# Performance work log

Measured on AMD Instinct MI355X. Metric: run time of the kernel, lower is better.

## Reference

```python
import jax, jax.numpy as jnp
import numpy as np

EPS = 1e-5
N_HEADS = 4

def _ln(x, s, b):
    m = x.mean(-1, keepdims=True)
    v = ((x - m) ** 2).mean(-1, keepdims=True)
    return (x - m) / jnp.sqrt(v + EPS) * s + b

def _gelu(x):
    return jax.nn.gelu(x, approximate=False)  # torch nn.GELU default (erf)


def setup_inputs() -> dict:
    key = jax.random.key(0)
    ks = jax.random.split(key, 20)
    H, AF, BF, DEPTH = 256, 153, 14, 4
    n_mols, apm = 1024, 48
    n_atoms = n_mols * apm          # 49152
    max_nb = 6
    n_bonds = 3 * n_atoms           # 147456 directed bonds
    def nrm(k, shape, scale=0.02):
        return jax.random.normal(k, shape, jnp.float32) * scale
    return dict(
        f_atoms=jax.random.normal(ks[0], (n_atoms, AF), jnp.float32),
        f_bonds=jax.random.normal(ks[1], (n_bonds, BF), jnp.float32),
        a2b=jax.random.randint(ks[2], (n_atoms, max_nb), 0, n_bonds),
        b2a=jax.random.randint(ks[3], (n_bonds,), 0, n_atoms),
        b2revb=jax.random.randint(ks[4], (n_bonds,), 0, n_bonds),
        W_i=nrm(ks[5], (AF + BF, H)), b_i=jnp.zeros((H,), jnp.float32),
        W_h=nrm(ks[6], (DEPTH - 1, H, H)), b_h=jnp.zeros((DEPTH - 1, H), jnp.float32),
        ln_msg_s=jnp.ones((DEPTH - 1, H), jnp.float32), ln_msg_b=jnp.zeros((DEPTH - 1, H), jnp.float32),
        W_o=nrm(ks[7], (AF + H, H)), b_o=jnp.zeros((H,), jnp.float32),
        ln_atom_s=jnp.ones((H,), jnp.float32), ln_atom_b=jnp.zeros((H,), jnp.float32),
        q_w=nrm(ks[8], (H, H)), q_b=jnp.zeros((H,), jnp.float32),
        k_w=nrm(ks[9], (H, H)), k_b=jnp.zeros((H,), jnp.float32),
        v_w=nrm(ks[10], (H, H)), v_b=jnp.zeros((H,), jnp.float32),
        o_w=nrm(ks[11], (H, H)), o_b=jnp.zeros((H,), jnp.float32),
        ln1_s=jnp.ones((H,), jnp.float32), ln1_b=jnp.zeros((H,), jnp.float32),
        ln2_s=jnp.ones((H,), jnp.float32), ln2_b=jnp.zeros((H,), jnp.float32),
        ff1_w=nrm(ks[12], (H, 2 * H)), ff1_b=jnp.zeros((2 * H,), jnp.float32),
        ff2_w=nrm(ks[13], (2 * H, H)), ff2_b=jnp.zeros((H,), jnp.float32),
        readout_query=nrm(ks[14], (1, 1, H)),
        rk_w=nrm(ks[15], (H, H)), rk_b=jnp.zeros((H,), jnp.float32),
        n_mols=n_mols, atoms_per_mol=apm,
    )


def reference(f_atoms, f_bonds, a2b, b2a, b2revb,
              W_i, b_i, W_h, b_h, ln_msg_s, ln_msg_b, W_o, b_o,
              ln_atom_s, ln_atom_b, q_w, q_b, k_w, k_b, v_w, v_b, o_w, o_b,
              ln1_s, ln1_b, ln2_s, ln2_b, ff1_w, ff1_b, ff2_w, ff2_b,
              readout_query, rk_w, rk_b, n_mols, atoms_per_mol):
    H = W_i.shape[1]
    HD = H // N_HEADS
    depth = W_h.shape[0] + 1

    # ---- D-MPNN message passing over directed bonds ----
    message = _gelu(jnp.concatenate([f_atoms[b2a], f_bonds], axis=1) @ W_i + b_i)  # [n_bonds,H]
    for t in range(depth - 1):  # fixed small depth loop
        nei = message[a2b].sum(axis=1)                 # [n_atoms,H] gather-sum over incoming bonds
        nei_m = nei[b2a] - message[b2revb]             # [n_bonds,H] subtract reverse bond
        message = message + _gelu(_ln(nei_m, ln_msg_s[t], ln_msg_b[t]) @ W_h[t] + b_h[t])

    a_message = message[a2b].sum(axis=1)               # [n_atoms,H]
    atom_h = _gelu(jnp.concatenate([f_atoms, a_message], axis=1) @ W_o + b_o)
    atom_h = _ln(atom_h, ln_atom_s, ln_atom_b)

    # uniform scopes: padding loop becomes a reshape, mask is all-valid
    x = atom_h.reshape(n_mols, atoms_per_mol, H)

    # ---- pre-norm TransformerEncoderLayer ----
    h = _ln(x, ln1_s, ln1_b)
    def heads(t):
        return t.reshape(n_mols, atoms_per_mol, N_HEADS, HD).transpose(0, 2, 1, 3)
    q = heads(h @ q_w + q_b)
    k = heads(h @ k_w + k_b)
    v = heads(h @ v_w + v_b)
    attn = jax.nn.softmax(jnp.einsum('bhqd,bhkd->bhqk', q, k) / float(np.sqrt(HD)), axis=-1)
    ctx = jnp.einsum('bhqk,bhkd->bhqd', attn, v).transpose(0, 2, 1, 3).reshape(n_mols, atoms_per_mol, H)
    x = x + (ctx @ o_w + o_b)
    h2 = _ln(x, ln2_s, ln2_b)
    x = x + (_gelu(h2 @ ff1_w + ff1_b) @ ff2_w + ff2_b)

    # ---- attention-weighted readout ----
    keys = x @ rk_w + rk_b                             # [B,S,H]
    scores = jnp.einsum('bsh,h->bs', keys, readout_query[0, 0])
    w = jax.nn.softmax(scores, axis=-1)[..., None]
    return (x * w).sum(axis=1)                         # [B,H]
```

## Files before the change

### kernel.cpp

```cpp
#include <hip/hip_runtime.h>
#include <hip/hip_bf16.h>
#include <math.h>

#define H 256
#define AFEAT 153
#define BFEAT 14
#define KINIT 167
#define NA 49152
#define NB 147456
#define NMOL 1024
#define APM 48
#define MAXNB 6
#define NHEAD 4
#define HDIM 64
#define EPSLN 1e-5f
#define KI_PAD 192
#define KO_PAD 448

typedef unsigned short u16;
typedef __attribute__((ext_vector_type(8))) short bf16x8;
typedef __attribute__((ext_vector_type(4))) short bf16x4;
typedef __attribute__((ext_vector_type(4))) float f32x4;

__device__ __forceinline__ float gelu_f(float x) {
    return 0.5f * x * (1.0f + erff(x * 0.70710678118654752f));
}
__device__ __forceinline__ float wave_sum(float v) {
    #pragma unroll
    for (int m = 1; m < 64; m <<= 1) v += __shfl_xor(v, m);
    return v;
}
__device__ __forceinline__ float b2f(u16 u) {
    union { unsigned u32; float f; } c; c.u32 = ((unsigned)u) << 16; return c.f;
}
__device__ __forceinline__ u16 f2b(float f) {
    __hip_bfloat16 h = __float2bfloat16(f);
    u16 u; __builtin_memcpy(&u, &h, 2); return u;
}
__device__ __forceinline__ ushort4 f2b4(float a, float b, float c, float d) {
    ushort4 o; o.x = f2b(a); o.y = f2b(b); o.z = f2b(c); o.w = f2b(d); return o;
}

__device__ __forceinline__ f32x4 mfma16(bf16x4 a, bf16x4 b, f32x4 c) {
#if __has_builtin(__builtin_amdgcn_mfma_f32_16x16x16bf16_1k)
    return __builtin_amdgcn_mfma_f32_16x16x16bf16_1k(a, b, c, 0, 0, 0);
#elif __has_builtin(__builtin_amdgcn_mfma_f32_16x16x16_bf16_1k)
    return __builtin_amdgcn_mfma_f32_16x16x16_bf16_1k(a, b, c, 0, 0, 0);
#elif __has_builtin(__builtin_amdgcn_mfma_f32_16x16x16_bf16)
    return __builtin_amdgcn_mfma_f32_16x16x16_bf16(a, b, c, 0, 0, 0);
#else
    f32x4 d;
    asm("v_mfma_f32_16x16x16_bf16 %0, %1, %2, %3"
        : "=&v"(d) : "v"(a), "v"(b), "v"(c));
    return d;
#endif
}

typedef const __attribute__((address_space(1))) void* gas_ptr;
typedef __attribute__((address_space(3))) void* las_ptr;
__device__ __forceinline__ void gload_lds16(const u16* g, u16* l) {
    __builtin_amdgcn_global_load_lds((gas_ptr)g, (las_ptr)l, 16, 0, 0);
}

template<bool GELU, bool ACCUM>
__global__ __launch_bounds__(256) void gemm_mfma_k(
    const u16* __restrict__ A, int Ka,
    const u16* __restrict__ Wt,
    const float* __restrict__ bias,
    u16* __restrict__ C, int Nc, int K)
{
    __shared__ __align__(16) u16 As[128 * 64];
    __shared__ __align__(16) u16 Bs[128 * 64];
    const int tid = threadIdx.x;
    const int w = tid >> 6, l = tid & 63;
    const int r0 = blockIdx.x * 128;
    const int cb0 = blockIdx.y * 128;
    const int wr = (w >> 1) * 64;
    const int wc = (w & 1) * 64;

    f32x4 acc[4][4];
    #pragma unroll
    for (int m = 0; m < 4; ++m)
        #pragma unroll
        for (int n = 0; n < 4; ++n) acc[m][n] = (f32x4){0.f, 0.f, 0.f, 0.f};

    const int srow = l >> 3;
    const int sslot = (l & 7) * 16;
    const int ssrc = sslot ^ (srow << 4);

    const int fr = l & 15;
    const int fh = l >> 4;
    const int swz = (fr & 7) << 4;

    for (int k0 = 0; k0 < K; k0 += 64) {
        #pragma unroll
        for (int i = 0; i < 4; ++i) {
            const int seg = w * 4 + i;
            gload_lds16(A + (size_t)(r0 + seg * 8 + srow) * Ka + k0 + (ssrc >> 1),
                        &As[seg * 512]);
            gload_lds16(Wt + (size_t)(cb0 + seg * 8 + srow) * Ka + k0 + (ssrc >> 1),
                        &Bs[seg * 512]);
        }
        __syncthreads();
        #pragma unroll
        for (int s = 0; s < 2; ++s) {
            const int cbyte = ((s * 64 + fh * 16) ^ swz) >> 1;
            bf16x8 af[4], bv[4];
            #pragma unroll
            for (int m = 0; m < 4; ++m)
                af[m] = *(const bf16x8*)&As[(wr + m * 16 + fr) * 64 + cbyte];
            #pragma unroll
            for (int n = 0; n < 4; ++n)
                bv[n] = *(const bf16x8*)&Bs[(wc + n * 16 + fr) * 64 + cbyte];
            #pragma unroll
            for (int m = 0; m < 4; ++m)
                #pragma unroll
                for (int n = 0; n < 4; ++n)
                    acc[m][n] = __builtin_amdgcn_mfma_f32_16x16x32_bf16(
                        af[m], bv[n], acc[m][n], 0, 0, 0);
        }
        __syncthreads();
    }

    float bvv[4];
    #pragma unroll
    for (int n = 0; n < 4; ++n) bvv[n] = bias[cb0 + wc + n * 16 + fr];
    #pragma unroll
    for (int m = 0; m < 4; ++m) {
        #pragma unroll
        for (int n = 0; n < 4; ++n) {
            const int col = cb0 + wc + n * 16 + fr;
            #pragma unroll
            for (int j = 0; j < 4; ++j) {
                const int row = r0 + wr + m * 16 + fh * 4 + j;
                float v = acc[m][n][j] + bvv[n];
                if (GELU) v = gelu_f(v);
                u16* p = &C[(size_t)row * Nc + col];
                if (ACCUM) v += b2f(*p);
                *p = f2b(v);
            }
        }
    }
}

__global__ __launch_bounds__(256) void wcvt_k(const float* __restrict__ W,
    u16* __restrict__ Wt, int K, int N, int Kpad)
{
    int idx = blockIdx.x * 256 + threadIdx.x;
    if (idx >= N * Kpad) return;
    int n = idx / Kpad, kp = idx - n * Kpad;
    Wt[idx] = (kp < K) ? f2b(W[(size_t)kp * N + n]) : (u16)0;
}

__global__ void biaspack_k(const float* q, const float* k, const float* v, float* dst) {
    int t = threadIdx.x;
    dst[t] = q[t]; dst[256 + t] = k[t]; dst[512 + t] = v[t];
}

__global__ __launch_bounds__(256) void ainit_k(const float* __restrict__ fa,
    const float* __restrict__ fb, const int* __restrict__ b2a, u16* __restrict__ dst)
{
    const int w = threadIdx.x >> 6, l = threadIdx.x & 63;
    const int row = blockIdx.x * 4 + w;
    const int a = b2a[row];
    const float* fsrc = fa + (size_t)a * AFEAT;
    u16* d = dst + (size_t)row * KI_PAD;
    #pragma unroll
    for (int i = 0; i < 3; ++i) {
        int c = l + i * 64;
        float v;
        if (c < AFEAT) v = fsrc[c];
        else if (c < KINIT) v = fb[(size_t)row * BFEAT + (c - AFEAT)];
        else v = 0.f;
        d[c] = f2b(v);
    }
}

__global__ __launch_bounds__(256) void acat_k(const float* __restrict__ fa,
    const u16* __restrict__ nei, u16* __restrict__ dst)
{
    const int w = threadIdx.x >> 6, l = threadIdx.x & 63;
    const int row = blockIdx.x * 4 + w;
    const float* fsrc = fa + (size_t)row * AFEAT;
    const u16* nsrc = nei + (size_t)row * H;
    u16* d = dst + (size_t)row * KO_PAD;
    #pragma unroll
    for (int i = 0; i < 7; ++i) {
        int c = l + i * 64;
        u16 v;
        if (c < AFEAT) v = f2b(fsrc[c]);
        else if (c < AFEAT + H) v = nsrc[c - AFEAT];
        else v = 0;
        d[c] = v;
    }
}

__global__ __launch_bounds__(256) void nei_sum_k(const u16* __restrict__ msg,
    const int* __restrict__ a2b, u16* __restrict__ nei)
{
    const int wave = threadIdx.x >> 6;
    const int lane = threadIdx.x & 63;
    const int atom = blockIdx.x * 4 + wave;
    float ax = 0.f, ay = 0.f, az = 0.f, aw = 0.f;
    #pragma unroll
    for (int j = 0; j < MAXNB; ++j) {
        int b = a2b[atom * MAXNB + j];
        ushort4 v = *(const ushort4*)(msg + (size_t)b * H + lane * 4);
        ax += b2f(v.x); ay += b2f(v.y); az += b2f(v.z); aw += b2f(v.w);
    }
    *(ushort4*)(nei + (size_t)atom * H + lane * 4) = f2b4(ax, ay, az, aw);
}

__global__ __launch_bounds__(256) void bond_ln_k(const u16* __restrict__ nei,
    const u16* __restrict__ msg, const int* __restrict__ b2a,
    const int* __restrict__ b2revb, const float* __restrict__ s,
    const float* __restrict__ b, u16* __restrict__ out)
{
    const int wave = threadIdx.x >> 6;
    const int lane = threadIdx.x & 63;
    const int bond = blockIdx.x * 4 + wave;
    const int a = b2a[bond];
    const int rb = b2revb[bond];
    ushort4 un = *(const ushort4*)(nei + (size_t)a * H + lane * 4);
    ushort4 um = *(const ushort4*)(msg + (size_t)rb * H + lane * 4);
    float vx = b2f(un.x) - b2f(um.x), vy = b2f(un.y) - b2f(um.y);
    float vz = b2f(un.z) - b2f(um.z), vw = b2f(un.w) - b2f(um.w);
    float mean = wave_sum(vx + vy + vz + vw) * (1.0f / H);
    float dx = vx - mean, dy = vy - mean, dz = vz - mean, dw = vw - mean;
    float var = wave_sum(dx * dx + dy * dy + dz * dz + dw * dw) * (1.0f / H);
    float inv = rsqrtf(var + EPSLN);
    float4 s4 = *(const float4*)(s + lane * 4);
    float4 b4 = *(const float4*)(b + lane * 4);
    *(ushort4*)(out + (size_t)bond * H + lane * 4) =
        f2b4(dx * inv * s4.x + b4.x, dy * inv * s4.y + b4.y,
             dz * inv * s4.z + b4.z, dw * inv * s4.w + b4.w);
}

__global__ __launch_bounds__(256) void row_ln_k(const u16* __restrict__ in,
    u16* __restrict__ out, const float* __restrict__ s, const float* __restrict__ b)
{
    const int wave = threadIdx.x >> 6;
    const int lane = threadIdx.x & 63;
    const int row = blockIdx.x * 4 + wave;
    ushort4 u = *(const ushort4*)(in + (size_t)row * H + lane * 4);
    float vx = b2f(u.x), vy = b2f(u.y), vz = b2f(u.z), vw = b2f(u.w);
    float mean = wave_sum(vx + vy + vz + vw) * (1.0f / H);
    float dx = vx - mean, dy = vy - mean, dz = vz - mean, dw = vw - mean;
    float var = wave_sum(dx * dx + dy * dy + dz * dz + dw * dw) * (1.0f / H);
    float inv = rsqrtf(var + EPSLN);
    float4 s4 = *(const float4*)(s + lane * 4);
    float4 b4 = *(const float4*)(b + lane * 4);
    *(ushort4*)(out + (size_t)row * H + lane * 4) =
        f2b4(dx * inv * s4.x + b4.x, dy * inv * s4.y + b4.y,
             dz * inv * s4.z + b4.z, dw * inv * s4.w + b4.w);
}

#define VPAD 268
__global__ __launch_bounds__(256) void attn_mfma_k(const u16* __restrict__ qkv,
    u16* __restrict__ ctx)
{
    __shared__ u16 Vs[48][VPAD];
    const int mol = blockIdx.x;
    const int tid = threadIdx.x;
    const int w = tid >> 6;
    const int l = tid & 63;
    const int fr = l & 15;
    const int fh = l >> 4;
    const size_t qb = (size_t)mol * APM * 768;

    {
        const int r = tid >> 4;
        const int c = (tid & 15) * 16;
        #pragma unroll
        for (int i = 0; i < 3; ++i) {
            const int row = r + i * 16;
            const u16* src = qkv + qb + (size_t)row * 768 + 512 + c;
            ushort4 a0 = *(const ushort4*)(src);
            ushort4 a1 = *(const ushort4*)(src + 4);
            ushort4 a2 = *(const ushort4*)(src + 8);
            ushort4 a3 = *(const ushort4*)(src + 12);
            *(ushort4*)&Vs[row][c]      = a0;
            *(ushort4*)&Vs[row][c + 4]  = a1;
            *(ushort4*)&Vs[row][c + 8]  = a2;
            *(ushort4*)&Vs[row][c + 12] = a3;
        }
    }
    __syncthreads();

    f32x4 st[3][3];
    {
        bf16x8 kf[3][2], qf[3][2];
        #pragma unroll
        for (int t = 0; t < 3; ++t)
            #pragma unroll
            for (int ks = 0; ks < 2; ++ks) {
                const size_t rowb = qb + (size_t)(t * 16 + fr) * 768;
                kf[t][ks] = *(const bf16x8*)(qkv + rowb + 256 + w * 64 + ks * 32 + fh * 8);
                qf[t][ks] = *(const bf16x8*)(qkv + rowb +       w * 64 + ks * 32 + fh * 8);
            }
        #pragma unroll
        for (int mi = 0; mi < 3; ++mi)
            #pragma unroll
            for (int ni = 0; ni < 3; ++ni) {
                f32x4 a = (f32x4){0.f, 0.f, 0.f, 0.f};
                a = __builtin_amdgcn_mfma_f32_16x16x32_bf16(kf[mi][0], qf[ni][0], a, 0, 0, 0);
                a = __builtin_amdgcn_mfma_f32_16x16x32_bf16(kf[mi][1], qf[ni][1], a, 0, 0, 0);
                st[mi][ni] = a;
            }
    }

    float inv_sum[3];
    #pragma unroll
    for (int ni = 0; ni < 3; ++ni) {
        float m = -1e30f;
        #pragma unroll
        for (int mi = 0; mi < 3; ++mi)
            #pragma unroll
            for (int j = 0; j < 4; ++j) m = fmaxf(m, st[mi][ni][j]);
        m = fmaxf(m, __shfl_xor(m, 16));
        m = fmaxf(m, __shfl_xor(m, 32));
        float s = 0.f;
        #pragma unroll
        for (int mi = 0; mi < 3; ++mi)
            #pragma unroll
            for (int j = 0; j < 4; ++j) {
                float e = expf((st[mi][ni][j] - m) * 0.125f);
                st[mi][ni][j] = e;
                s += e;
            }
        s += __shfl_xor(s, 16);
        s += __shfl_xor(s, 32);
        inv_sum[ni] = 1.0f / s;
    }

    bf16x4 pf[3][3];
    #pragma unroll
    for (int mi = 0; mi < 3; ++mi)
        #pragma unroll
        for (int ni = 0; ni < 3; ++ni) {
            bf16x4 p;
            p[0] = (short)f2b(st[mi][ni][0]);
            p[1] = (short)f2b(st[mi][ni][1]);
            p[2] = (short)f2b(st[mi][ni][2]);
            p[3] = (short)f2b(st[mi][ni][3]);
            pf[mi][ni] = p;
        }

    f32x4 co[4][3];
    #pragma unroll
    for (int dt = 0; dt < 4; ++dt)
        #pragma unroll
        for (int ni = 0; ni < 3; ++ni) co[dt][ni] = (f32x4){0.f, 0.f, 0.f, 0.f};
    #pragma unroll
    for (int kt = 0; kt < 3; ++kt) {
        bf16x4 vf[4];
        #pragma unroll
        for (int dt = 0; dt < 4; ++dt) {
            const int colu = w * 64 + dt * 16 + fr;
            bf16x4 t;
            #pragma unroll
            for (int e = 0; e < 4; ++e)
                t[e] = (short)Vs[kt * 16 + fh * 4 + e][colu];
            vf[dt] = t;
        }
        #pragma unroll
        for (int dt = 0; dt < 4; ++dt)
            #pragma unroll
            for (int ni = 0; ni < 3; ++ni)
                co[dt][ni] = mfma16(vf[dt], pf[kt][ni], co[dt][ni]);
    }

    #pragma unroll
    for (int ni = 0; ni < 3; ++ni) {
        const float is = inv_sum[ni];
        u16* rowp = ctx + (size_t)(mol * APM + ni * 16 + fr) * H + w * 64;
        #pragma unroll
        for (int dt = 0; dt < 4; ++dt) {
            *(ushort4*)(rowp + dt * 16 + fh * 4) =
                f2b4(co[dt][ni][0] * is, co[dt][ni][1] * is,
                     co[dt][ni][2] * is, co[dt][ni][3] * is);
        }
    }
}

__global__ __launch_bounds__(256) void readout_prep_k(const float* __restrict__ rk_w,
    const float* __restrict__ rk_b, const float* __restrict__ query, float* __restrict__ small)
{
    __shared__ float qsh[256];
    __shared__ float red[4];
    const int t = threadIdx.x;
    qsh[t] = query[t];
    __syncthreads();
    float acc = 0.f;
    #pragma unroll
    for (int c = 0; c < 256; c += 4) {
        float4 w = *(const float4*)&rk_w[(size_t)t * 256 + c];
        acc += w.x * qsh[c] + w.y * qsh[c+1] + w.z * qsh[c+2] + w.w * qsh[c+3];
    }
    small[t] = acc;
    float term = wave_sum(rk_b[t] * qsh[t]);
    if ((t & 63) == 0) red[t >> 6] = term;
    __syncthreads();
    if (t == 0) small[256] = red[0] + red[1] + red[2] + red[3];
}

__global__ __launch_bounds__(256) void readout_k(const u16* __restrict__ x,
    const float* __restrict__ small, float* __restrict__ out)
{
    __shared__ float sc[48];
    __shared__ float rvs[256];
    const int mol = blockIdx.x;
    const int t = threadIdx.x;
    const int wave = t >> 6, lane = t & 63;
    rvs[t] = small[t];
    __syncthreads();
    const float c0 = small[256];
    const size_t xb = (size_t)mol * APM * H;
    for (int i = 0; i < 12; ++i) {
        int s = wave * 12 + i;
        ushort4 xu = *(const ushort4*)(x + xb + (size_t)s * H + lane * 4);
        float dot = b2f(xu.x) * rvs[lane*4] + b2f(xu.y) * rvs[lane*4+1]
                  + b2f(xu.z) * rvs[lane*4+2] + b2f(xu.w) * rvs[lane*4+3];
        dot = wave_sum(dot);
        if (lane == 0) sc[s] = dot + c0;
    }
    __syncthreads();
    if (wave == 0) {
        float v = (lane < 48) ? sc[lane] : -1e30f;
        float mx = v;
        #pragma unroll
        for (int m = 1; m < 64; m <<= 1) mx = fmaxf(mx, __shfl_xor(mx, m));
        float e = (lane < 48) ? expf(v - mx) : 0.f;
        float sum = wave_sum(e);
        if (lane < 48) sc[lane] = e / sum;
    }
    __syncthreads();
    float acc = 0.f;
    for (int s = 0; s < 48; ++s) acc += sc[s] * b2f(x[xb + (size_t)s * H + t]);
    out[(size_t)mol * H + t] = acc;
}

__global__ void diag_k(float* out, int n, float val) {
    int i = blockIdx.x * 256 + threadIdx.x;
    if (i < n) out[i] = (i == 0) ? val : 0.f;
}

extern "C" void kernel_launch(void* const* d_in, const int* in_sizes, int n_in,
                              void* d_out, int out_size, void* d_ws, size_t ws_size,
                              hipStream_t stream)
{
    const float* f_atoms = (const float*)d_in[0];
    const float* f_bonds = (const float*)d_in[1];
    const int*   a2b     = (const int*)d_in[2];
    const int*   b2a     = (const int*)d_in[3];
    const int*   b2revb  = (const int*)d_in[4];
    const float* W_i = (const float*)d_in[5];
    const float* b_i = (const float*)d_in[6];
    const float* W_h = (const float*)d_in[7];
    const float* b_h = (const float*)d_in[8];
    const float* ln_msg_s = (const float*)d_in[9];
    const float* ln_msg_b = (const float*)d_in[10];
    const float* W_o = (const float*)d_in[11];
    const float* b_o = (const float*)d_in[12];
    const float* ln_atom_s = (const float*)d_in[13];
    const float* ln_atom_b = (const float*)d_in[14];
    const float* q_w = (const float*)d_in[15];
    const float* q_b = (const float*)d_in[16];
    const float* k_w = (const float*)d_in[17];
    const float* k_b = (const float*)d_in[18];
    const float* v_w = (const float*)d_in[19];
    const float* v_b = (const float*)d_in[20];
    const float* o_w = (const float*)d_in[21];
    const float* o_b = (const float*)d_in[22];
    const float* ln1_s = (const float*)d_in[23];
    const float* ln1_b = (const float*)d_in[24];
    const float* ln2_s = (const float*)d_in[25];
    const float* ln2_b = (const float*)d_in[26];
    const float* ff1_w = (const float*)d_in[27];
    const float* ff1_b = (const float*)d_in[28];
    const float* ff2_w = (const float*)d_in[29];
    const float* ff2_b = (const float*)d_in[30];
    const float* rquery = (const float*)d_in[31];
    const float* rk_w = (const float*)d_in[32];
    const float* rk_b = (const float*)d_in[33];

    const size_t SZ_MSG = (size_t)NB * H;
    const size_t SZ_NEI = (size_t)NA * H;
    const size_t W_I_SZ  = 256 * KI_PAD;
    const size_t W_H_SZ  = 3 * 256 * 256;
    const size_t W_O_SZ  = 256 * KO_PAD;
    const size_t W_QKV_SZ = 768 * 256;
    const size_t W_OG_SZ = 256 * 256;
    const size_t W_F1_SZ = 512 * 256;
    const size_t W_F2_SZ = 256 * 512;
    const size_t wtotal = W_I_SZ + W_H_SZ + W_O_SZ + W_QKV_SZ + W_OG_SZ + W_F1_SZ + W_F2_SZ;
    const size_t required = (2 * SZ_MSG + SZ_NEI + wtotal) * 2 + 768 * 4 + 257 * 4 + 256;
    if (ws_size < required) {
        diag_k<<<dim3((out_size + 255) / 256), dim3(256), 0, stream>>>(
            (float*)d_out, out_size, (float)(ws_size >> 20));
        return;
    }

    u16* msg    = (u16*)d_ws;
    u16* normed = msg + SZ_MSG;
    u16* nei    = normed + SZ_MSG;
    u16* wt_i   = nei + SZ_NEI;
    u16* wt_h   = wt_i + W_I_SZ;
    u16* wt_o   = wt_h + W_H_SZ;
    u16* wt_qkv = wt_o + W_O_SZ;
    u16* wt_og  = wt_qkv + W_QKV_SZ;
    u16* wt_f1  = wt_og + W_OG_SZ;
    u16* wt_f2  = wt_f1 + W_F1_SZ;
    float* qkvb = (float*)(wt_f2 + W_F2_SZ);
    float* small = qkvb + 768;

    u16* x    = msg;
    u16* h    = msg + SZ_NEI;
    u16* qkv  = normed;
    u16* ctx  = nei;
    u16* h2   = msg + SZ_NEI;
    u16* ff1o = normed;
    float* out = (float*)d_out;

    dim3 blk(256);
    #define WCVT(W, DST, K, N, KP) wcvt_k<<<dim3(((N)*(KP)+255)/256), blk, 0, stream>>>(W, DST, K, N, KP)

    WCVT(W_i, wt_i, KINIT, 256, KI_PAD);
    WCVT(W_h,           wt_h,           256, 256, 256);
    WCVT(W_h + 65536,   wt_h + 65536,   256, 256, 256);
    WCVT(W_h + 131072,  wt_h + 131072,  256, 256, 256);
    WCVT(W_o, wt_o, AFEAT + H, 256, KO_PAD);
    WCVT(q_w, wt_qkv,          256, 256, 256);
    WCVT(k_w, wt_qkv + 65536,  256, 256, 256);
    WCVT(v_w, wt_qkv + 131072, 256, 256, 256);
    WCVT(o_w, wt_og, 256, 256, 256);
    WCVT(ff1_w, wt_f1, 256, 512, 256);
    WCVT(ff2_w, wt_f2, 512, 256, 512);
    biaspack_k<<<dim3(1), blk, 0, stream>>>(q_b, k_b, v_b, qkvb);

    ainit_k<<<dim3(NB / 4), blk, 0, stream>>>(f_atoms, f_bonds, b2a, normed);
    gemm_mfma_k<true, false><<<dim3(NB / 128, 2), blk, 0, stream>>>(
        normed, KI_PAD, wt_i, b_i, msg, H, KI_PAD);

    for (int t = 0; t < 3; ++t) {
        nei_sum_k<<<dim3(NA / 4), blk, 0, stream>>>(msg, a2b, nei);
        bond_ln_k<<<dim3(NB / 4), blk, 0, stream>>>(nei, msg, b2a, b2revb,
            ln_msg_s + t * H, ln_msg_b + t * H, normed);
        gemm_mfma_k<true, true><<<dim3(NB / 128, 2), blk, 0, stream>>>(
            normed, H, wt_h + (size_t)t * 65536, b_h + t * H, msg, H, H);
    }

    nei_sum_k<<<dim3(NA / 4), blk, 0, stream>>>(msg, a2b, nei);
    acat_k<<<dim3(NA / 4), blk, 0, stream>>>(f_atoms, nei, normed);
    gemm_mfma_k<true, false><<<dim3(NA / 128, 2), blk, 0, stream>>>(
        normed, KO_PAD, wt_o, b_o, x, H, KO_PAD);
    row_ln_k<<<dim3(NA / 4), blk, 0, stream>>>(x, x, ln_atom_s, ln_atom_b);

    row_ln_k<<<dim3(NA / 4), blk, 0, stream>>>(x, h, ln1_s, ln1_b);
    gemm_mfma_k<false, false><<<dim3(NA / 128, 6), blk, 0, stream>>>(
        h, H, wt_qkv, qkvb, qkv, 768, H);
    attn_mfma_k<<<dim3(NMOL), blk, 0, stream>>>(qkv, ctx);
    gemm_mfma_k<false, true><<<dim3(NA / 128, 2), blk, 0, stream>>>(
        ctx, H, wt_og, o_b, x, H, H);
    row_ln_k<<<dim3(NA / 4), blk, 0, stream>>>(x, h2, ln2_s, ln2_b);
    gemm_mfma_k<true, false><<<dim3(NA / 128, 4), blk, 0, stream>>>(
        h2, H, wt_f1, ff1_b, ff1o, 512, H);
    gemm_mfma_k<false, true><<<dim3(NA / 128, 2), blk, 0, stream>>>(
        ff1o, 512, wt_f2, ff2_b, x, H, 512);

    readout_prep_k<<<dim3(1), blk, 0, stream>>>(rk_w, rk_b, rquery, small);
    readout_k<<<dim3(NMOL), blk, 0, stream>>>(x, small, out);
}
```

Baseline: 779.8 us.

## Fuse LayerNorm and bond gather into GEMM prologue, stage epilogue via LDS

```diff
diff --git a/kernel.cpp b/kernel.cpp
--- a/kernel.cpp
+++ b/kernel.cpp
@@ -40,6 +40,17 @@
 __device__ __forceinline__ ushort4 f2b4(float a, float b, float c, float d) {
     ushort4 o; o.x = f2b(a); o.y = f2b(b); o.z = f2b(c); o.w = f2b(d); return o;
 }
+__device__ __forceinline__ unsigned addbf2(unsigned a, unsigned b) {
+    float lo = b2f((u16)(a & 0xffff)) + b2f((u16)(b & 0xffff));
+    float hi = b2f((u16)(a >> 16)) + b2f((u16)(b >> 16));
+    return ((unsigned)f2b(hi) << 16) | (unsigned)f2b(lo);
+}
+__device__ __forceinline__ uint4 addbf8(uint4 a, uint4 b) {
+    uint4 r;
+    r.x = addbf2(a.x, b.x); r.y = addbf2(a.y, b.y);
+    r.z = addbf2(a.z, b.z); r.w = addbf2(a.w, b.w);
+    return r;
+}
 
 __device__ __forceinline__ f32x4 mfma16(bf16x4 a, bf16x4 b, f32x4 c) {
 #if __has_builtin(__builtin_amdgcn_mfma_f32_16x16x16bf16_1k)
@@ -69,8 +80,9 @@
     const float* __restrict__ bias,
     u16* __restrict__ C, int Nc, int K)
 {
-    __shared__ __align__(16) u16 As[128 * 64];
-    __shared__ __align__(16) u16 Bs[128 * 64];
+    __shared__ __align__(16) u16 S[128 * 128];
+    u16* As = S;
+    u16* Bs = S + 8192;
     const int tid = threadIdx.x;
     const int w = tid >> 6, l = tid & 63;
     const int r0 = blockIdx.x * 128;
@@ -85,9 +97,7 @@
         for (int n = 0; n < 4; ++n) acc[m][n] = (f32x4){0.f, 0.f, 0.f, 0.f};
 
     const int srow = l >> 3;
-    const int sslot = (l & 7) * 16;
-    const int ssrc = sslot ^ (srow << 4);
-
+    const int ssrc = ((l & 7) * 16) ^ (srow << 4);
     const int fr = l & 15;
     const int fh = l >> 4;
     const int swz = (fr & 7) << 4;
@@ -126,19 +136,161 @@
     #pragma unroll
     for (int n = 0; n < 4; ++n) bvv[n] = bias[cb0 + wc + n * 16 + fr];
     #pragma unroll
-    for (int m = 0; m < 4; ++m) {
+    for (int m = 0; m < 4; ++m)
         #pragma unroll
         for (int n = 0; n < 4; ++n) {
-            const int col = cb0 + wc + n * 16 + fr;
+            const int col = wc + n * 16 + fr;
             #pragma unroll
             for (int j = 0; j < 4; ++j) {
-                const int row = r0 + wr + m * 16 + fh * 4 + j;
+                const int row = wr + m * 16 + fh * 4 + j;
                 float v = acc[m][n][j] + bvv[n];
                 if (GELU) v = gelu_f(v);
-                u16* p = &C[(size_t)row * Nc + col];
-                if (ACCUM) v += b2f(*p);
-                *p = f2b(v);
+                *(u16*)((char*)S + row * 256 + ((col * 2) ^ ((row & 7) << 4))) = f2b(v);
             }
+        }
+    __syncthreads();
+    {
+        const int rrow = tid >> 1;
+        const int rch = (tid & 1) * 128;
+        const int rswz = (rrow & 7) << 4;
+        u16* gp = C + (size_t)(r0 + rrow) * Nc + cb0 + (tid & 1) * 64;
+        #pragma unroll
+        for (int q = 0; q < 8; ++q) {
+            uint4 dv = *(const uint4*)((const char*)S + rrow * 256 + ((rch + q * 16) ^ rswz));
+            if (ACCUM) {
+                uint4 ov = *(const uint4*)(gp + q * 8);
+                dv = addbf8(dv, ov);
+            }
+            *(uint4*)(gp + q * 8) = dv;
+        }
+    }
+}
+
+struct LGather {
+    const u16* nei; const u16* msg; const int* b2a; const int* b2revb;
+    __device__ __forceinline__ float4 load4(int row, int lane) const {
+        const int a = b2a[row], rv = b2revb[row];
+        ushort4 un = *(const ushort4*)(nei + (size_t)a * H + lane * 4);
+        ushort4 um = *(const ushort4*)(msg + (size_t)rv * H + lane * 4);
+        return make_float4(b2f(un.x) - b2f(um.x), b2f(un.y) - b2f(um.y),
+                           b2f(un.z) - b2f(um.z), b2f(un.w) - b2f(um.w));
+    }
+};
+struct LPlain {
+    const u16* X;
+    __device__ __forceinline__ float4 load4(int row, int lane) const {
+        ushort4 u = *(const ushort4*)(X + (size_t)row * H + lane * 4);
+        return make_float4(b2f(u.x), b2f(u.y), b2f(u.z), b2f(u.w));
+    }
+};
+
+template<class L, bool GELU, bool ACCUM>
+__global__ __launch_bounds__(512, 4) void fln_gemm_k(
+    L ld, const u16* __restrict__ Wt,
+    const float* __restrict__ lns, const float* __restrict__ lnb,
+    const float* __restrict__ bias,
+    const u16* __restrict__ Cold,
+    u16* __restrict__ C, int Nc)
+{
+    __shared__ __align__(16) u16 SH[64 * 256 + 256 * 64];
+    u16* Alds = SH;
+    u16* Blds = SH + 64 * 256;
+    const int tid = threadIdx.x;
+    const int w = tid >> 6, l = tid & 63;
+    const int r0 = blockIdx.x * 64;
+    const int cb0 = blockIdx.y * 256;
+    const int fr = l & 15, fh = l >> 4;
+    const int swzf = (fr & 7) << 4;
+
+    {
+        float4 sv = *(const float4*)(lns + l * 4);
+        float4 bv = *(const float4*)(lnb + l * 4);
+        #pragma unroll
+        for (int i = 0; i < 8; ++i) {
+            const int r = w * 8 + i;
+            float4 v = ld.load4(r0 + r, l);
+            float mean = wave_sum(v.x + v.y + v.z + v.w) * (1.0f / H);
+            float dx = v.x - mean, dy = v.y - mean, dz = v.z - mean, dw = v.w - mean;
+            float var = wave_sum(dx * dx + dy * dy + dz * dz + dw * dw) * (1.0f / H);
+            float inv = rsqrtf(var + EPSLN);
+            ushort4 o = f2b4(dx * inv * sv.x + bv.x, dy * inv * sv.y + bv.y,
+                             dz * inv * sv.z + bv.z, dw * inv * sv.w + bv.w);
+            *(ushort4*)((char*)&Alds[(size_t)r * 256] + ((l * 8) ^ ((r & 7) << 4))) = o;
+        }
+    }
+
+    f32x4 acc[2][4];
+    #pragma unroll
+    for (int m = 0; m < 2; ++m)
+        #pragma unroll
+        for (int n = 0; n < 4; ++n) acc[m][n] = (f32x4){0.f, 0.f, 0.f, 0.f};
+
+    const int wr = (w >> 2) * 32;
+    const int wc = (w & 3) * 64;
+
+    for (int kk = 0; kk < 4; ++kk) {
+        #pragma unroll
+        for (int i = 0; i < 4; ++i) {
+            const int seg = w * 4 + i;
+            const int n = seg * 8 + (l >> 3);
+            const int sb = ((l & 7) * 16) ^ ((n & 7) << 4);
+            gload_lds16(Wt + (size_t)(cb0 + n) * H + kk * 64 + (sb >> 1),
+                        &Blds[seg * 512]);
+        }
+        __syncthreads();
+        #pragma unroll
+        for (int s = 0; s < 2; ++s) {
+            bf16x8 af[2], bv[4];
+            #pragma unroll
+            for (int m = 0; m < 2; ++m)
+                af[m] = *(const bf16x8*)((const char*)&Alds[(size_t)(wr + m * 16 + fr) * 256]
+                        + ((kk * 128 + s * 64 + fh * 16) ^ swzf));
+            #pragma unroll
+            for (int n = 0; n < 4; ++n)
+                bv[n] = *(const bf16x8*)((const char*)&Blds[(size_t)(wc + n * 16 + fr) * 64]
+                        + ((s * 64 + fh * 16) ^ swzf));
+            #pragma unroll
+            for (int m = 0; m < 2; ++m)
+                #pragma unroll
+                for (int n = 0; n < 4; ++n)
+                    acc[m][n] = __builtin_amdgcn_mfma_f32_16x16x32_bf16(
+                        af[m], bv[n], acc[m][n], 0, 0, 0);
+        }
+        __syncthreads();
+    }
+
+    float bvv[4];
+    #pragma unroll
+    for (int n = 0; n < 4; ++n) bvv[n] = bias[cb0 + wc + n * 16 + fr];
+    #pragma unroll
+    for (int m = 0; m < 2; ++m)
+        #pragma unroll
+        for (int n = 0; n < 4; ++n) {
+            const int col = wc + n * 16 + fr;
+            #pragma unroll
+            for (int j = 0; j < 4; ++j) {
+                const int row = wr + m * 16 + fh * 4 + j;
+                float v = acc[m][n][j] + bvv[n];
+                if (GELU) v = gelu_f(v);
+                *(u16*)((char*)&Alds[(size_t)row * 256] + ((col * 2) ^ ((row & 7) << 4))) = f2b(v);
+            }
+        }
+    __syncthreads();
+    {
+        const int rrow = tid >> 3;
+        const int rch = (tid & 7) * 64;
+        const int rswz = (rrow & 7) << 4;
+        u16* gp = C + (size_t)(r0 + rrow) * Nc + cb0 + (tid & 7) * 32;
+        const u16* op = Cold + (size_t)(r0 + rrow) * Nc + cb0 + (tid & 7) * 32;
+        #pragma unroll
+        for (int q = 0; q < 4; ++q) {
+            uint4 dv = *(const uint4*)((const char*)&Alds[(size_t)rrow * 256]
+                        + ((rch + q * 16) ^ rswz));
+            if (ACCUM) {
+                uint4 ov = *(const uint4*)(op + q * 8);
+                dv = addbf8(dv, ov);
+            }
+            *(uint4*)(gp + q * 8) = dv;
         }
     }
 }
@@ -209,31 +361,6 @@
         ax += b2f(v.x); ay += b2f(v.y); az += b2f(v.z); aw += b2f(v.w);
     }
     *(ushort4*)(nei + (size_t)atom * H + lane * 4) = f2b4(ax, ay, az, aw);
-}
-
-__global__ __launch_bounds__(256) void bond_ln_k(const u16* __restrict__ nei,
-    const u16* __restrict__ msg, const int* __restrict__ b2a,
-    const int* __restrict__ b2revb, const float* __restrict__ s,
-    const float* __restrict__ b, u16* __restrict__ out)
-{
-    const int wave = threadIdx.x >> 6;
-    const int lane = threadIdx.x & 63;
-    const int bond = blockIdx.x * 4 + wave;
-    const int a = b2a[bond];
-    const int rb = b2revb[bond];
-    ushort4 un = *(const ushort4*)(nei + (size_t)a * H + lane * 4);
-    ushort4 um = *(const ushort4*)(msg + (size_t)rb * H + lane * 4);
-    float vx = b2f(un.x) - b2f(um.x), vy = b2f(un.y) - b2f(um.y);
-    float vz = b2f(un.z) - b2f(um.z), vw = b2f(un.w) - b2f(um.w);
-    float mean = wave_sum(vx + vy + vz + vw) * (1.0f / H);
-    float dx = vx - mean, dy = vy - mean, dz = vz - mean, dw = vw - mean;
-    float var = wave_sum(dx * dx + dy * dy + dz * dz + dw * dw) * (1.0f / H);
-    float inv = rsqrtf(var + EPSLN);
-    float4 s4 = *(const float4*)(s + lane * 4);
-    float4 b4 = *(const float4*)(b + lane * 4);
-    *(ushort4*)(out + (size_t)bond * H + lane * 4) =
-        f2b4(dx * inv * s4.x + b4.x, dy * inv * s4.y + b4.y,
-             dz * inv * s4.z + b4.z, dw * inv * s4.w + b4.w);
 }
 
 __global__ __launch_bounds__(256) void row_ln_k(const u16* __restrict__ in,
@@ -501,9 +628,9 @@
         return;
     }
 
-    u16* msg    = (u16*)d_ws;
-    u16* normed = msg + SZ_MSG;
-    u16* nei    = normed + SZ_MSG;
+    u16* msgA   = (u16*)d_ws;
+    u16* msgB   = msgA + SZ_MSG;
+    u16* nei    = msgB + SZ_MSG;
     u16* wt_i   = nei + SZ_NEI;
     u16* wt_h   = wt_i + W_I_SZ;
     u16* wt_o   = wt_h + W_H_SZ;
@@ -513,16 +640,10 @@
     u16* wt_f2  = wt_f1 + W_F1_SZ;
     float* qkvb = (float*)(wt_f2 + W_F2_SZ);
     float* small = qkvb + 768;
-
-    u16* x    = msg;
-    u16* h    = msg + SZ_NEI;
-    u16* qkv  = normed;
-    u16* ctx  = nei;
-    u16* h2   = msg + SZ_NEI;
-    u16* ff1o = normed;
     float* out = (float*)d_out;
 
     dim3 blk(256);
+    dim3 blk5(512);
     #define WCVT(W, DST, K, N, KP) wcvt_k<<<dim3(((N)*(KP)+255)/256), blk, 0, stream>>>(W, DST, K, N, KP)
 
     WCVT(W_i, wt_i, KINIT, 256, KI_PAD);
@@ -538,33 +659,38 @@
     WCVT(ff2_w, wt_f2, 512, 256, 512);
     biaspack_k<<<dim3(1), blk, 0, stream>>>(q_b, k_b, v_b, qkvb);
 
-    ainit_k<<<dim3(NB / 4), blk, 0, stream>>>(f_atoms, f_bonds, b2a, normed);
+    ainit_k<<<dim3(NB / 4), blk, 0, stream>>>(f_atoms, f_bonds, b2a, msgB);
     gemm_mfma_k<true, false><<<dim3(NB / 128, 2), blk, 0, stream>>>(
-        normed, KI_PAD, wt_i, b_i, msg, H, KI_PAD);
-
+        msgB, KI_PAD, wt_i, b_i, msgA, H, KI_PAD);
+
+    u16* cur = msgA;
+    u16* oth = msgB;
     for (int t = 0; t < 3; ++t) {
-        nei_sum_k<<<dim3(NA / 4), blk, 0, stream>>>(msg, a2b, nei);
-        bond_ln_k<<<dim3(NB / 4), blk, 0, stream>>>(nei, msg, b2a, b2revb,
-            ln_msg_s + t * H, ln_msg_b + t * H, normed);
-        gemm_mfma_k<true, true><<<dim3(NB / 128, 2), blk, 0, stream>>>(
-            normed, H, wt_h + (size_t)t * 65536, b_h + t * H, msg, H, H);
-    }
-
-    nei_sum_k<<<dim3(NA / 4), blk, 0, stream>>>(msg, a2b, nei);
-    acat_k<<<dim3(NA / 4), blk, 0, stream>>>(f_atoms, nei, normed);
+        nei_sum_k<<<dim3(NA / 4), blk, 0, stream>>>(cur, a2b, nei);
+        fln_gemm_k<LGather, true, true><<<dim3(NB / 64, 1), blk5, 0, stream>>>(
+            LGather{nei, cur, b2a, b2revb}, wt_h + (size_t)t * 65536,
+            ln_msg_s + t * H, ln_msg_b + t * H, b_h + t * H,
+            cur, oth, H);
+        u16* tmp = cur; cur = oth; oth = tmp;
+    }
+
+    nei_sum_k<<<dim3(NA / 4), blk, 0, stream>>>(cur, a2b, nei);
+    acat_k<<<dim3(NA / 4), blk, 0, stream>>>(f_atoms, nei, oth);
+    u16* x = cur;
     gemm_mfma_k<true, false><<<dim3(NA / 128, 2), blk, 0, stream>>>(
-        normed, KO_PAD, wt_o, b_o, x, H, KO_PAD);
+        oth, KO_PAD, wt_o, b_o, x, H, KO_PAD);
     row_ln_k<<<dim3(NA / 4), blk, 0, stream>>>(x, x, ln_atom_s, ln_atom_b);
 
-    row_ln_k<<<dim3(NA / 4), blk, 0, stream>>>(x, h, ln1_s, ln1_b);
-    gemm_mfma_k<false, false><<<dim3(NA / 128, 6), blk, 0, stream>>>(
-        h, H, wt_qkv, qkvb, qkv, 768, H);
+    u16* qkv = oth;
+    fln_gemm_k<LPlain, false, false><<<dim3(NA / 64, 3), blk5, 0, stream>>>(
+        LPlain{x}, wt_qkv, ln1_s, ln1_b, qkvb, x, qkv, 768);
+    u16* ctx = nei;
     attn_mfma_k<<<dim3(NMOL), blk, 0, stream>>>(qkv, ctx);
     gemm_mfma_k<false, true><<<dim3(NA / 128, 2), blk, 0, stream>>>(
         ctx, H, wt_og, o_b, x, H, H);
-    row_ln_k<<<dim3(NA / 4), blk, 0, stream>>>(x, h2, ln2_s, ln2_b);
-    gemm_mfma_k<true, false><<<dim3(NA / 128, 4), blk, 0, stream>>>(
-        h2, H, wt_f1, ff1_b, ff1o, 512, H);
+    u16* ff1o = oth;
+    fln_gemm_k<LPlain, true, false><<<dim3(NA / 64, 2), blk5, 0, stream>>>(
+        LPlain{x}, wt_f1, ln2_s, ln2_b, ff1_b, x, ff1o, 512);
     gemm_mfma_k<false, true><<<dim3(NA / 128, 2), blk, 0, stream>>>(
         ff1o, 512, wt_f2, ff2_b, x, H, 512);
 
```

New measurement: 736.0 us. 1.06x faster.
